# Kernel optimization log

Hardware: AMD Instinct MI355X
Metric: run time of the kernel (lower is better)

The kernel has to match this reference:

```python
import jax, jax.numpy as jnp
import numpy as np

GRID_SIZE = 64
THRESHOLD = 1.0
SIGMA = 1.5
K_SHARP = 2.0


def _gaussian_kernel(sigma):
    ksize = max(int(4 * sigma) | 1, 3)
    x = jnp.arange(ksize, dtype=jnp.float32) - ksize // 2
    g1d = jnp.exp(-x ** 2 / (2.0 * sigma ** 2))
    g2d = g1d[None, :] * g1d[:, None]
    g2d = g2d / g2d.sum()
    return g2d[None, None]  # (1,1,k,k) OIHW


def setup_inputs() -> dict:
    key = jax.random.key(0)
    k1, k2, k3, k4 = jax.random.split(key, 4)
    B, V, P, N, MAXP = 4, 512, 8192, 2000, 8
    positions = jax.random.uniform(k1, (B, V, 2), dtype=jnp.float32) * 2.0 - 1.0
    pin_offsets = jax.random.normal(k2, (P, 2), dtype=jnp.float32) * 0.05
    net_to_pin = jax.random.randint(k3, (N, MAXP), 0, P, dtype=jnp.int32)
    pin_to_macro = jax.random.randint(k4, (P,), 0, V, dtype=jnp.int32)
    return {"positions": positions, "pin_offsets": pin_offsets,
            "net_to_pin": net_to_pin, "pin_to_macro": pin_to_macro}


def reference(positions, pin_offsets, net_to_pin, pin_to_macro):
    B = positions.shape[0]
    M = GRID_SIZE
    num_nets = net_to_pin.shape[0]

    # pin positions: (B, P, 2) -- no rotation (rotation_onehot=None branch)
    pin_pos = positions[:, pin_to_macro, :] + pin_offsets[None]

    # per-net bounding boxes over valid pins
    valid = net_to_pin >= 0                                  # (N, maxp)
    safe_idx = jnp.maximum(net_to_pin, 0)
    net_pin_pos = pin_pos[:, safe_idx, :]                    # (B, N, maxp, 2)
    mask = valid[None, :, :, None]
    bbox_max = jnp.max(jnp.where(mask, net_pin_pos, -1e9), axis=2)  # (B, N, 2)
    bbox_min = jnp.min(jnp.where(mask, net_pin_pos, 1e9), axis=2)

    # to grid coordinates
    bbox_max_g = (bbox_max + 1.0) * 0.5 * (M - 1)
    bbox_min_g = (bbox_min + 1.0) * 0.5 * (M - 1)

    # soft rectangular indicators on the MxM grid
    gx = jnp.arange(M, dtype=jnp.float32)
    grid_x, grid_y = jnp.meshgrid(gx, gx, indexing="xy")     # (M, M)
    grid_x = grid_x[None, None]                               # (1,1,M,M)
    grid_y = grid_y[None, None]
    x_min = bbox_min_g[..., 0][..., None, None]               # (B,N,1,1)
    x_max = bbox_max_g[..., 0][..., None, None]
    y_min = bbox_min_g[..., 1][..., None, None]
    y_max = bbox_max_g[..., 1][..., None, None]

    in_x = jax.nn.sigmoid(K_SHARP * (grid_x - x_min + 0.5)) * \
           jax.nn.sigmoid(K_SHARP * (x_max - grid_x + 0.5))
    in_y = jax.nn.sigmoid(K_SHARP * (grid_y - y_min + 0.5)) * \
           jax.nn.sigmoid(K_SHARP * (y_max - grid_y + 0.5))
    indicator = in_x * in_y                                    # (B,N,M,M)

    bbox_size = jnp.maximum((x_max - x_min + 1.0) * (y_max - y_min + 1.0), 1.0)
    rudy = jnp.sum(indicator / bbox_size, axis=1, keepdims=True)  # (B,1,M,M)

    # gaussian smoothing (SAME padding)
    kernel = _gaussian_kernel(SIGMA)
    pad = kernel.shape[-1] // 2
    rudy_smooth = jax.lax.conv_general_dilated(
        rudy, kernel, window_strides=(1, 1),
        padding=((pad, pad), (pad, pad)),
        dimension_numbers=("NCHW", "OIHW", "NCHW"))

    overflow = jax.nn.relu(rudy_smooth - THRESHOLD)
    penalty = jnp.sum(overflow ** 2, axis=(1, 2, 3))           # (B,)
    return penalty, rudy_smooth
```

## Files before the change

### kernel.cpp

```cpp
#include <hip/hip_runtime.h>

#define GRID   64
#define BATCH  4
#define NV     512
#define NP     8192
#define NNET   2000
#define MAXPIN 8
#define NB     32
#define NCHUNK 63

__device__ __forceinline__ float sigmoidf_fast(float z) {
    return 1.0f / (1.0f + __expf(-z));
}

__global__ __launch_bounds__(256)
void rudy_accum_kernel(const float* __restrict__ positions,
                       const float* __restrict__ pin_offsets,
                       const int*   __restrict__ net_to_pin,
                       const int*   __restrict__ pin_to_macro,
                       float* __restrict__ rudy) {
    const int chunk = blockIdx.x;
    const int b     = blockIdx.y;
    const int t     = threadIdx.x;

    __shared__ float s_inx[NB][GRID];
    __shared__ float s_iny[NB][GRID];
    __shared__ float s_xmin[NB], s_xmax[NB], s_ymin[NB], s_ymax[NB], s_inv[NB];

    {
        const int nl = t >> 3;
        const int j  = t & 7;
        const int n  = chunk * NB + nl;
        int pi = (n < NNET) ? net_to_pin[n * MAXPIN + j] : -1;
        int sp = pi > 0 ? pi : 0;
        int v  = pin_to_macro[sp];
        float px = positions[(b * NV + v) * 2 + 0] + pin_offsets[sp * 2 + 0];
        float py = positions[(b * NV + v) * 2 + 1] + pin_offsets[sp * 2 + 1];
        bool valid = pi >= 0;
        float xmx = valid ? px : -1e9f;
        float xmn = valid ? px :  1e9f;
        float ymx = valid ? py : -1e9f;
        float ymn = valid ? py :  1e9f;
        #pragma unroll
        for (int off = 1; off < 8; off <<= 1) {
            xmx = fmaxf(xmx, __shfl_xor(xmx, off, 64));
            xmn = fminf(xmn, __shfl_xor(xmn, off, 64));
            ymx = fmaxf(ymx, __shfl_xor(ymx, off, 64));
            ymn = fminf(ymn, __shfl_xor(ymn, off, 64));
        }
        if (j == 0) {
            float xming = (xmn + 1.0f) * 31.5f;
            float xmaxg = (xmx + 1.0f) * 31.5f;
            float yming = (ymn + 1.0f) * 31.5f;
            float ymaxg = (ymx + 1.0f) * 31.5f;
            float size = fmaxf((xmaxg - xming + 1.0f) * (ymaxg - yming + 1.0f), 1.0f);
            s_xmin[nl] = xming; s_xmax[nl] = xmaxg;
            s_ymin[nl] = yming; s_ymax[nl] = ymaxg;
            s_inv[nl]  = 1.0f / size;
        }
    }
    __syncthreads();

    #pragma unroll
    for (int i = 0; i < 16; ++i) {
        int v     = i * 256 + t;
        int n     = v >> 7;
        int rem   = v & 127;
        int which = rem >> 6;
        int coord = rem & 63;
        float c  = (float)coord;
        float lo = which ? s_ymin[n] : s_xmin[n];
        float hi = which ? s_ymax[n] : s_xmax[n];
        float val = sigmoidf_fast(2.0f * (c - lo + 0.5f)) *
                    sigmoidf_fast(2.0f * (hi - c + 0.5f));
        if (which) s_iny[n][coord] = val; else s_inx[n][coord] = val;
    }
    __syncthreads();

    const int lane = t & 63;
    const int w    = t >> 6;
    float acc[16];
    #pragma unroll
    for (int k = 0; k < 16; ++k) acc[k] = 0.0f;

    for (int n = 0; n < NB; ++n) {
        float xv = s_inx[n][lane] * s_inv[n];
        const float4* iny4 = (const float4*)&s_iny[n][w * 16];
        #pragma unroll
        for (int k4 = 0; k4 < 4; ++k4) {
            float4 yv = iny4[k4];
            acc[k4 * 4 + 0] += yv.x * xv;
            acc[k4 * 4 + 1] += yv.y * xv;
            acc[k4 * 4 + 2] += yv.z * xv;
            acc[k4 * 4 + 3] += yv.w * xv;
        }
    }

    float* dst = rudy + b * (GRID * GRID);
    #pragma unroll
    for (int k = 0; k < 16; ++k) {
        int cell = (w * 16 + k) * GRID + lane;
        atomicAdd(&dst[cell], acc[k]);
    }
}

__global__ __launch_bounds__(256)
void smooth_penalty_kernel(const float* __restrict__ rudy,
                           float* __restrict__ out_penalty,
                           float* __restrict__ out_smooth) {
    const int b = blockIdx.x;
    const int t = threadIdx.x;

    __shared__ float tile[GRID * GRID];
    __shared__ float tmp [GRID * GRID];
    __shared__ float red[4];

    float g[7];
    {
        float s = 0.0f;
        #pragma unroll
        for (int i = 0; i < 7; ++i) {
            float d = (float)(i - 3);
            g[i] = expf(-d * d / 4.5f);
            s += g[i];
        }
        float inv = 1.0f / s;
        #pragma unroll
        for (int i = 0; i < 7; ++i) g[i] *= inv;
    }

    const float* src = rudy + b * GRID * GRID;
    #pragma unroll
    for (int k = 0; k < 16; ++k) tile[k * 256 + t] = src[k * 256 + t];
    __syncthreads();

    #pragma unroll
    for (int k = 0; k < 16; ++k) {
        int c = k * 256 + t;
        int y = c >> 6, x = c & 63;
        float s = 0.0f;
        #pragma unroll
        for (int d = -3; d <= 3; ++d) {
            int xx = x + d;
            if (xx >= 0 && xx < GRID) s += g[d + 3] * tile[y * GRID + xx];
        }
        tmp[c] = s;
    }
    __syncthreads();

    float local = 0.0f;
    #pragma unroll
    for (int k = 0; k < 16; ++k) {
        int c = k * 256 + t;
        int y = c >> 6, x = c & 63;
        float s = 0.0f;
        #pragma unroll
        for (int d = -3; d <= 3; ++d) {
            int yy = y + d;
            if (yy >= 0 && yy < GRID) s += g[d + 3] * tmp[yy * GRID + x];
        }
        out_smooth[b * GRID * GRID + c] = s;
        float ov = s - 1.0f;
        ov = ov > 0.0f ? ov : 0.0f;
        local += ov * ov;
    }

    #pragma unroll
    for (int off = 32; off > 0; off >>= 1) local += __shfl_down(local, off, 64);
    if ((t & 63) == 0) red[t >> 6] = local;
    __syncthreads();
    if (t == 0) out_penalty[b] = red[0] + red[1] + red[2] + red[3];
}

extern "C" void kernel_launch(void* const* d_in, const int* in_sizes, int n_in,
                              void* d_out, int out_size, void* d_ws, size_t ws_size,
                              hipStream_t stream) {
    const float* positions    = (const float*)d_in[0];
    const float* pin_offsets  = (const float*)d_in[1];
    const int*   net_to_pin   = (const int*)d_in[2];
    const int*   pin_to_macro = (const int*)d_in[3];
    float* out  = (float*)d_out;
    float* rudy = (float*)d_ws;

    hipMemsetAsync(d_ws, 0, BATCH * GRID * GRID * sizeof(float), stream);
    rudy_accum_kernel<<<dim3(NCHUNK, BATCH), 256, 0, stream>>>(
        positions, pin_offsets, net_to_pin, pin_to_macro, rudy);
    smooth_penalty_kernel<<<BATCH, 256, 0, stream>>>(rudy, out, out + BATCH);
}
```

Measured before the change: 76.79 us.

## Replace atomic accumulation with per-block partial grids and fused reduce-smooth kernel

Drops the memset and global atomicAdd accumulation. Each block now loops over several 32-net chunks and writes its own partial 64x64 grid, and a 1024-thread kernel sums the partials before smoothing. This removes atomic contention and one launch, but cuts the first kernel from 252 blocks to at most 64, so far fewer CUs are active. The inverse bbox size is also folded into the x indicator when it is computed.

```diff
diff --git a/kernel.cpp b/kernel.cpp
--- a/kernel.cpp
+++ b/kernel.cpp
@@ -1,119 +1,127 @@
 #include <hip/hip_runtime.h>
 
 #define GRID   64
+#define CELLS  (GRID * GRID)
 #define BATCH  4
 #define NV     512
-#define NP     8192
 #define NNET   2000
 #define MAXPIN 8
 #define NB     32
-#define NCHUNK 63
+#define NPART_MAX 16
 
 __device__ __forceinline__ float sigmoidf_fast(float z) {
     return 1.0f / (1.0f + __expf(-z));
 }
 
 __global__ __launch_bounds__(256)
-void rudy_accum_kernel(const float* __restrict__ positions,
-                       const float* __restrict__ pin_offsets,
-                       const int*   __restrict__ net_to_pin,
-                       const int*   __restrict__ pin_to_macro,
-                       float* __restrict__ rudy) {
-    const int chunk = blockIdx.x;
-    const int b     = blockIdx.y;
-    const int t     = threadIdx.x;
+void rudy_partial_kernel(const float* __restrict__ positions,
+                         const float* __restrict__ pin_offsets,
+                         const int*   __restrict__ net_to_pin,
+                         const int*   __restrict__ pin_to_macro,
+                         float* __restrict__ partial,
+                         int subs) {
+    const int pb = blockIdx.x;
+    const int b  = blockIdx.y;
+    const int t  = threadIdx.x;
 
     __shared__ float s_inx[NB][GRID];
     __shared__ float s_iny[NB][GRID];
     __shared__ float s_xmin[NB], s_xmax[NB], s_ymin[NB], s_ymax[NB], s_inv[NB];
 
-    {
-        const int nl = t >> 3;
-        const int j  = t & 7;
-        const int n  = chunk * NB + nl;
-        int pi = (n < NNET) ? net_to_pin[n * MAXPIN + j] : -1;
-        int sp = pi > 0 ? pi : 0;
-        int v  = pin_to_macro[sp];
-        float px = positions[(b * NV + v) * 2 + 0] + pin_offsets[sp * 2 + 0];
-        float py = positions[(b * NV + v) * 2 + 1] + pin_offsets[sp * 2 + 1];
-        bool valid = pi >= 0;
-        float xmx = valid ? px : -1e9f;
-        float xmn = valid ? px :  1e9f;
-        float ymx = valid ? py : -1e9f;
-        float ymn = valid ? py :  1e9f;
-        #pragma unroll
-        for (int off = 1; off < 8; off <<= 1) {
-            xmx = fmaxf(xmx, __shfl_xor(xmx, off, 64));
-            xmn = fminf(xmn, __shfl_xor(xmn, off, 64));
-            ymx = fmaxf(ymx, __shfl_xor(ymx, off, 64));
-            ymn = fminf(ymn, __shfl_xor(ymn, off, 64));
-        }
-        if (j == 0) {
-            float xming = (xmn + 1.0f) * 31.5f;
-            float xmaxg = (xmx + 1.0f) * 31.5f;
-            float yming = (ymn + 1.0f) * 31.5f;
-            float ymaxg = (ymx + 1.0f) * 31.5f;
-            float size = fmaxf((xmaxg - xming + 1.0f) * (ymaxg - yming + 1.0f), 1.0f);
-            s_xmin[nl] = xming; s_xmax[nl] = xmaxg;
-            s_ymin[nl] = yming; s_ymax[nl] = ymaxg;
-            s_inv[nl]  = 1.0f / size;
-        }
-    }
-    __syncthreads();
-
-    #pragma unroll
-    for (int i = 0; i < 16; ++i) {
-        int v     = i * 256 + t;
-        int n     = v >> 7;
-        int rem   = v & 127;
-        int which = rem >> 6;
-        int coord = rem & 63;
-        float c  = (float)coord;
-        float lo = which ? s_ymin[n] : s_xmin[n];
-        float hi = which ? s_ymax[n] : s_xmax[n];
-        float val = sigmoidf_fast(2.0f * (c - lo + 0.5f)) *
-                    sigmoidf_fast(2.0f * (hi - c + 0.5f));
-        if (which) s_iny[n][coord] = val; else s_inx[n][coord] = val;
-    }
-    __syncthreads();
-
     const int lane = t & 63;
     const int w    = t >> 6;
+
     float acc[16];
     #pragma unroll
     for (int k = 0; k < 16; ++k) acc[k] = 0.0f;
 
-    for (int n = 0; n < NB; ++n) {
-        float xv = s_inx[n][lane] * s_inv[n];
-        const float4* iny4 = (const float4*)&s_iny[n][w * 16];
-        #pragma unroll
-        for (int k4 = 0; k4 < 4; ++k4) {
-            float4 yv = iny4[k4];
-            acc[k4 * 4 + 0] += yv.x * xv;
-            acc[k4 * 4 + 1] += yv.y * xv;
-            acc[k4 * 4 + 2] += yv.z * xv;
-            acc[k4 * 4 + 3] += yv.w * xv;
-        }
-    }
-
-    float* dst = rudy + b * (GRID * GRID);
-    #pragma unroll
-    for (int k = 0; k < 16; ++k) {
-        int cell = (w * 16 + k) * GRID + lane;
-        atomicAdd(&dst[cell], acc[k]);
-    }
-}
-
-__global__ __launch_bounds__(256)
-void smooth_penalty_kernel(const float* __restrict__ rudy,
-                           float* __restrict__ out_penalty,
-                           float* __restrict__ out_smooth) {
+    const int base = pb * subs * NB;
+
+    for (int sub = 0; sub < subs; ++sub) {
+        const int n0 = base + sub * NB;
+
+        {
+            const int nl = t >> 3;
+            const int j  = t & 7;
+            const int n  = n0 + nl;
+            int pi = (n < NNET) ? net_to_pin[n * MAXPIN + j] : -1;
+            int sp = pi > 0 ? pi : 0;
+            int v  = pin_to_macro[sp];
+            float px = positions[(b * NV + v) * 2 + 0] + pin_offsets[sp * 2 + 0];
+            float py = positions[(b * NV + v) * 2 + 1] + pin_offsets[sp * 2 + 1];
+            bool valid = pi >= 0;
+            float xmx = valid ? px : -1e9f;
+            float xmn = valid ? px :  1e9f;
+            float ymx = valid ? py : -1e9f;
+            float ymn = valid ? py :  1e9f;
+            #pragma unroll
+            for (int off = 1; off < 8; off <<= 1) {
+                xmx = fmaxf(xmx, __shfl_xor(xmx, off, 64));
+                xmn = fminf(xmn, __shfl_xor(xmn, off, 64));
+                ymx = fmaxf(ymx, __shfl_xor(ymx, off, 64));
+                ymn = fminf(ymn, __shfl_xor(ymn, off, 64));
+            }
+            if (j == 0) {
+                float xming = (xmn + 1.0f) * 31.5f;
+                float xmaxg = (xmx + 1.0f) * 31.5f;
+                float yming = (ymn + 1.0f) * 31.5f;
+                float ymaxg = (ymx + 1.0f) * 31.5f;
+                float size = fmaxf((xmaxg - xming + 1.0f) * (ymaxg - yming + 1.0f), 1.0f);
+                s_xmin[nl] = xming; s_xmax[nl] = xmaxg;
+                s_ymin[nl] = yming; s_ymax[nl] = ymaxg;
+                s_inv[nl]  = 1.0f / size;
+            }
+        }
+        __syncthreads();
+
+        #pragma unroll
+        for (int i = 0; i < 16; ++i) {
+            int vv    = i * 256 + t;
+            int n     = vv >> 7;
+            int rem   = vv & 127;
+            int which = rem >> 6;
+            int coord = rem & 63;
+            float c  = (float)coord;
+            float lo = which ? s_ymin[n] : s_xmin[n];
+            float hi = which ? s_ymax[n] : s_xmax[n];
+            float val = sigmoidf_fast(2.0f * (c - lo + 0.5f)) *
+                        sigmoidf_fast(2.0f * (hi - c + 0.5f));
+            if (which) s_iny[n][coord] = val;
+            else       s_inx[n][coord] = val * s_inv[n];
+        }
+        __syncthreads();
+
+        for (int n = 0; n < NB; ++n) {
+            float xv = s_inx[n][lane];
+            const float4* iny4 = (const float4*)&s_iny[n][w * 16];
+            #pragma unroll
+            for (int k4 = 0; k4 < 4; ++k4) {
+                float4 yv = iny4[k4];
+                acc[k4 * 4 + 0] += yv.x * xv;
+                acc[k4 * 4 + 1] += yv.y * xv;
+                acc[k4 * 4 + 2] += yv.z * xv;
+                acc[k4 * 4 + 3] += yv.w * xv;
+            }
+        }
+    }
+
+    float* dst = partial + ((size_t)b * gridDim.x + pb) * CELLS;
+    #pragma unroll
+    for (int k = 0; k < 16; ++k)
+        dst[(w * 16 + k) * GRID + lane] = acc[k];
+}
+
+__global__ __launch_bounds__(1024)
+void reduce_smooth_kernel(const float* __restrict__ partial,
+                          float* __restrict__ out_penalty,
+                          float* __restrict__ out_smooth,
+                          int npart) {
     const int b = blockIdx.x;
     const int t = threadIdx.x;
 
-    __shared__ float tile[GRID * GRID];
-    __shared__ float tmp [GRID * GRID];
-    __shared__ float red[4];
+    __shared__ float tile[CELLS];
+    __shared__ float tmp [CELLS];
+    __shared__ float red [16];
 
     float g[7];
     {
@@ -129,14 +137,19 @@
         for (int i = 0; i < 7; ++i) g[i] *= inv;
     }
 
-    const float* src = rudy + b * GRID * GRID;
-    #pragma unroll
-    for (int k = 0; k < 16; ++k) tile[k * 256 + t] = src[k * 256 + t];
+    const float4* src = (const float4*)(partial + (size_t)b * npart * CELLS);
+    float4 a = {0.0f, 0.0f, 0.0f, 0.0f};
+    #pragma unroll 4
+    for (int p = 0; p < npart; ++p) {
+        float4 v = src[p * (CELLS / 4) + t];
+        a.x += v.x; a.y += v.y; a.z += v.z; a.w += v.w;
+    }
+    ((float4*)tile)[t] = a;
     __syncthreads();
 
     #pragma unroll
-    for (int k = 0; k < 16; ++k) {
-        int c = k * 256 + t;
+    for (int i = 0; i < 4; ++i) {
+        int c = i * 1024 + t;
         int y = c >> 6, x = c & 63;
         float s = 0.0f;
         #pragma unroll
@@ -150,8 +163,8 @@
 
     float local = 0.0f;
     #pragma unroll
-    for (int k = 0; k < 16; ++k) {
-        int c = k * 256 + t;
+    for (int i = 0; i < 4; ++i) {
+        int c = i * 1024 + t;
         int y = c >> 6, x = c & 63;
         float s = 0.0f;
         #pragma unroll
@@ -159,7 +172,7 @@
             int yy = y + d;
             if (yy >= 0 && yy < GRID) s += g[d + 3] * tmp[yy * GRID + x];
         }
-        out_smooth[b * GRID * GRID + c] = s;
+        out_smooth[b * CELLS + c] = s;
         float ov = s - 1.0f;
         ov = ov > 0.0f ? ov : 0.0f;
         local += ov * ov;
@@ -169,7 +182,12 @@
     for (int off = 32; off > 0; off >>= 1) local += __shfl_down(local, off, 64);
     if ((t & 63) == 0) red[t >> 6] = local;
     __syncthreads();
-    if (t == 0) out_penalty[b] = red[0] + red[1] + red[2] + red[3];
+    if (t == 0) {
+        float s = 0.0f;
+        #pragma unroll
+        for (int i = 0; i < 16; ++i) s += red[i];
+        out_penalty[b] = s;
+    }
 }
 
 extern "C" void kernel_launch(void* const* d_in, const int* in_sizes, int n_in,
@@ -179,11 +197,16 @@
     const float* pin_offsets  = (const float*)d_in[1];
     const int*   net_to_pin   = (const int*)d_in[2];
     const int*   pin_to_macro = (const int*)d_in[3];
-    float* out  = (float*)d_out;
-    float* rudy = (float*)d_ws;
-
-    hipMemsetAsync(d_ws, 0, BATCH * GRID * GRID * sizeof(float), stream);
-    rudy_accum_kernel<<<dim3(NCHUNK, BATCH), 256, 0, stream>>>(
-        positions, pin_offsets, net_to_pin, pin_to_macro, rudy);
-    smooth_penalty_kernel<<<BATCH, 256, 0, stream>>>(rudy, out, out + BATCH);
-}
+    float* out     = (float*)d_out;
+    float* partial = (float*)d_ws;
+
+    int npart = (int)(ws_size / ((size_t)BATCH * CELLS * sizeof(float)));
+    if (npart > NPART_MAX) npart = NPART_MAX;
+    if (npart < 1) npart = 1;
+    int nets_per_block = (NNET + npart - 1) / npart;
+    int subs = (nets_per_block + NB - 1) / NB;
+
+    rudy_partial_kernel<<<dim3(npart, BATCH), 256, 0, stream>>>(
+        positions, pin_offsets, net_to_pin, pin_to_macro, partial, subs);
+    reduce_smooth_kernel<<<BATCH, 1024, 0, stream>>>(partial, out, out + BATCH, npart);
+}
```

Result: slower. 85.05 us (+10.7%).
